# Kernel tuning notes

Hardware: AMD Instinct MI355X
Metric: run time of the kernel (lower is better)

The kernel has to match this reference:

```python
import jax, jax.numpy as jnp
import numpy as np
import itertools

COS_THRES = 0.5
TEMP = 0.1
EPS = 1e-06
NUM_MODALS = 3


def _cosine_sim(t1, t2, l1, l2, eps=EPS):
    # t1:[B1,D], t2:[B2,D], l1:[B1,1], l2:[B2,1] -> [B1,B2]
    return jnp.matmul(t1, t2.T) / jnp.maximum(jnp.matmul(l1, l2.T), eps)


def _filtered_infonce(m1, m2, cos_thres=COS_THRES, temp=TEMP, eps=EPS):
    # m1, m2: [B, D]
    B = m1.shape[0]
    l1 = jnp.sqrt(jnp.sum(m1 * m1, axis=-1, keepdims=True))
    l2 = jnp.sqrt(jnp.sum(m2 * m2, axis=-1, keepdims=True))
    cross = _cosine_sim(m1, m2, l1, l2, eps) / temp          # [B,B] logits
    s1 = _cosine_sim(m1, m1, l1, l1, eps)
    s2 = _cosine_sim(m2, m2, l2, l2, eps)
    mask = (s1 <= cos_thres) | (s2 <= cos_thres)
    mask = mask | jnp.eye(B, dtype=bool)                      # diagonal always kept
    # masked row-wise cross entropy with label i == diagonal.
    # Excluding masked columns then re-indexing the label (torch loop) is
    # equivalent to a masked softmax over the full row with label on the diag.
    neg_inf = jnp.asarray(-jnp.inf, cross.dtype)
    logits = jnp.where(mask, cross, neg_inf)
    lse = jax.nn.logsumexp(logits, axis=-1)                   # [B]
    loss_i = lse - jnp.diagonal(cross)                        # [B]
    valid = jnp.sum(mask, axis=-1) > 1                        # rows with >1 candidates
    count = jnp.sum(valid)
    total = jnp.sum(jnp.where(valid, loss_i, 0.0))
    return jnp.where(count > 0, total / jnp.maximum(count, 1), 0.0)


def setup_inputs() -> dict:
    key = jax.random.key(0)
    all_features = jax.random.normal(key, (NUM_MODALS, 4096, 1024), dtype=jnp.float32)
    return {"all_features": all_features}


def reference(all_features) -> jnp.ndarray:
    # CMCLoss with main_modal_idx=None: InfoNCE over all modal pairs.
    n_modals = all_features.shape[0]
    error = 0.0
    num_components = 0
    for i, j in itertools.combinations(range(n_modals), 2):
        error = error + _filtered_infonce(all_features[i], all_features[j])
        num_components += 1
    return error / num_components
```

## Files before the change

### kernel.cpp

```cpp
#include <hip/hip_runtime.h>
#include <stdint.h>
#include <math.h>

typedef float fx4 __attribute__((ext_vector_type(4)));
typedef float fx16 __attribute__((ext_vector_type(16)));
typedef int   ix4 __attribute__((ext_vector_type(4)));
typedef int   ix8 __attribute__((ext_vector_type(8)));

#define NB 4096
#define ND 1024
#define CEPS 1e-6f
#define CTHR 0.5f
#define NTT 16


__device__ __forceinline__ void gload16(const void* g, void* l) {
  __builtin_amdgcn_global_load_lds(
      (const __attribute__((address_space(1))) uint32_t*)(uintptr_t)g,
      (__attribute__((address_space(3))) uint32_t*)(uint32_t)(uintptr_t)l,
      16, 0, 0);
}

__device__ __forceinline__ ix8 ldfrag8(const char* p0, const char* p1) {
  const ix4 lo = *(const ix4*)p0;
  const ix4 hi = *(const ix4*)p1;
  ix8 r;
  r[0] = lo[0]; r[1] = lo[1]; r[2] = lo[2]; r[3] = lo[3];
  r[4] = hi[0]; r[5] = hi[1]; r[6] = hi[2]; r[7] = hi[3];
  return r;
}

#define MFMAS(A, B, C) \
  __builtin_amdgcn_mfma_scale_f32_32x32x64_f8f6f4((A), (B), (C), 0, 0, 0, 127, 0, 127)


__global__ __launch_bounds__(256) void cmc_convert(
    const float* __restrict__ in, uint8_t* __restrict__ xf8,
    float* __restrict__ lnorm) {
  const int row = blockIdx.x;
  const int tid = threadIdx.x;
  const fx4 v = *(const fx4*)(in + (size_t)row * ND + tid * 4);
  int pk = __builtin_amdgcn_cvt_pk_fp8_f32(v[0], v[1], 0, false);
  pk = __builtin_amdgcn_cvt_pk_fp8_f32(v[2], v[3], pk, true);
  ((int*)(xf8 + (size_t)row * ND))[tid] = pk;
  float ss = v[0]*v[0] + v[1]*v[1] + v[2]*v[2] + v[3]*v[3];
  #pragma unroll
  for (int d = 1; d < 64; d <<= 1) ss += __shfl_xor(ss, d);
  __shared__ float sred[4];
  if ((tid & 63) == 0) sred[tid >> 6] = ss;
  __syncthreads();
  if (tid == 0) lnorm[row] = sqrtf(sred[0] + sred[1] + sred[2] + sred[3]);
}


__device__ __forceinline__ void gram128_f8(
    const uint8_t* __restrict__ Xi, const uint8_t* __restrict__ Xj,
    int rb, int cb, char* smem, int tid, fx16 (&acc)[2][2]) {
  const int l = tid & 63, w = tid >> 6;
  const int wr = w >> 1, wc = w & 1;
  const int srow = tid >> 2;
  const int scol = (((tid & 3) ^ ((tid >> 3) & 3)) << 4);
  const uint8_t* gA0 = Xi + (size_t)(rb + srow) * ND + scol;
  const uint8_t* gA1 = Xi + (size_t)(rb + 64 + srow) * ND + scol;
  const uint8_t* gB0 = Xj + (size_t)(cb + srow) * ND + scol;
  const uint8_t* gB1 = Xj + (size_t)(cb + 64 + srow) * ND + scol;
  char* dA0 = smem + tid * 16;
  char* dA1 = smem + 4096 + tid * 16;
  char* dB0 = smem + 8192 + tid * 16;
  char* dB1 = smem + 12288 + tid * 16;

  const int swzl = ((l >> 1) & 3) << 4;
  const int kb = (l >> 5) * 32;
  const int c0 = kb ^ swzl;
  const int c1 = (kb + 16) ^ swzl;
  const char* rdA = smem + (wr * 64 + (l & 31)) * 64;
  const char* rdB = smem + 8192 + (wc * 64 + (l & 31)) * 64;

  #pragma unroll
  for (int m = 0; m < 2; ++m)
    #pragma unroll
    for (int n = 0; n < 2; ++n)
      #pragma unroll
      for (int e = 0; e < 16; ++e) acc[m][n][e] = 0.f;

  #pragma unroll 1
  for (int t = 0; t < NTT; ++t) {
    const int k0 = t * 64;
    gload16(gA0 + k0, dA0);
    gload16(gA1 + k0, dA1);
    gload16(gB0 + k0, dB0);
    gload16(gB1 + k0, dB1);
    __syncthreads();
    ix8 A[2], B[2];
    #pragma unroll
    for (int m = 0; m < 2; ++m)
      A[m] = ldfrag8(rdA + m * 2048 + c0, rdA + m * 2048 + c1);
    #pragma unroll
    for (int n = 0; n < 2; ++n)
      B[n] = ldfrag8(rdB + n * 2048 + c0, rdB + n * 2048 + c1);
    #pragma unroll
    for (int m = 0; m < 2; ++m)
      #pragma unroll
      for (int n = 0; n < 2; ++n)
        acc[m][n] = MFMAS(A[m], B[n], acc[m][n]);
    __syncthreads();
  }
}


__global__ __launch_bounds__(256, 3) void cmc_selfmask(
    const uint8_t* __restrict__ xf8, const float* __restrict__ lnorm,
    uint32_t* __restrict__ maskw) {
  __shared__ __align__(16) char smem[16384];
  const int md = blockIdx.z;
  const int bx = blockIdx.x, by = blockIdx.y;
  if (by > bx) return;
  const int rb = by * 128, cb = bx * 128;
  const int tid = threadIdx.x;
  const int l = tid & 63, w = tid >> 6;
  const int wr = w >> 1, wc = w & 1;

  const uint8_t* X = xf8 + (size_t)md * NB * ND;
  fx16 acc[2][2];
  gram128_f8(X, X, rb, cb, smem, tid, acc);

  uint32_t* tile = (uint32_t*)smem;
  float* Lr = (float*)(smem + 2048);
  float* Lc = (float*)(smem + 2560 + 512);
  if (tid < 128) {
    Lr[tid] = lnorm[md * NB + rb + tid];
    Lc[tid] = lnorm[md * NB + cb + tid];
  }
  __syncthreads();

  #pragma unroll
  for (int m = 0; m < 2; ++m)
    #pragma unroll
    for (int r = 0; r < 16; ++r) {
      const int rl0 = wr * 64 + m * 32 + (r & 3) + 8 * (r >> 2);
      const float Lrv = Lr[rl0 + 4 * (l >> 5)];
      #pragma unroll
      for (int n = 0; n < 2; ++n) {
        const int cl = wc * 64 + n * 32 + (l & 31);
        const float cv = acc[m][n][r] / fmaxf(Lrv * Lc[cl], CEPS);
        const uint64_t b = __ballot(cv <= CTHR);
        if (l == 0)  tile[(rl0 + 0) * 4 + wc * 2 + n] = (uint32_t)b;
        if (l == 32) tile[(rl0 + 4) * 4 + wc * 2 + n] = (uint32_t)(b >> 32);
      }
    }
  __syncthreads();

  for (int t = tid; t < 512; t += 256) {
    const int row = t >> 2, wd = t & 3;
    maskw[((size_t)md * NB + rb + row) * 128 + (cb >> 5) + wd] = tile[t];
  }
  if (by != bx) {
    for (int t = tid; t < 512; t += 256) {
      const int crow = t & 127;
      const int wp = t >> 7;
      uint32_t wv = 0;
      #pragma unroll
      for (int r = 0; r < 32; ++r) {
        const uint32_t bit = (tile[(wp * 32 + r) * 4 + (crow >> 5)] >> (crow & 31)) & 1u;
        wv |= bit << r;
      }
      maskw[((size_t)md * NB + cb + crow) * 128 + (rb >> 5) + wp] = wv;
    }
  }
}


__global__ __launch_bounds__(256, 3) void cmc_pair(
    const uint8_t* __restrict__ xf8, const float* __restrict__ lnorm,
    const uint32_t* __restrict__ maskw,
    float* __restrict__ sumexp, float* __restrict__ diagv) {
  __shared__ __align__(16) char smem[16384];
  const int p = blockIdx.z;
  const int mi = (p == 2) ? 1 : 0;
  const int mj = (p == 0) ? 1 : 2;
  const int rb = blockIdx.y * 128;
  const int cb = blockIdx.x * 128;
  const int tid = threadIdx.x;
  const int l = tid & 63, w = tid >> 6;
  const int wr = w >> 1, wc = w & 1;

  const uint8_t* Xi = xf8 + (size_t)mi * NB * ND;
  const uint8_t* Xj = xf8 + (size_t)mj * NB * ND;

  fx16 acc[2][2];
  gram128_f8(Xi, Xj, rb, cb, smem, tid, acc);

  uint32_t* Mt = (uint32_t*)smem;
  float* Lri = (float*)(smem + 4096);
  float* Lcj = (float*)(smem + 4608 + 512);
  for (int t = tid; t < 512; t += 256) {
    const int row = t >> 2, wd = t & 3;
    Mt[t]       = maskw[((size_t)mi * NB + rb + row) * 128 + (cb >> 5) + wd];
    Mt[512 + t] = maskw[((size_t)mj * NB + rb + row) * 128 + (cb >> 5) + wd];
  }
  if (tid < 128) {
    Lri[tid] = lnorm[mi * NB + rb + tid];
    Lcj[tid] = lnorm[mj * NB + cb + tid];
  }
  __syncthreads();

  #pragma unroll
  for (int m = 0; m < 2; ++m)
    #pragma unroll
    for (int r = 0; r < 16; ++r) {
      const int rl = wr * 64 + m * 32 + (r & 3) + 8 * (r >> 2) + 4 * (l >> 5);
      const int rg = rb + rl;
      const float Lrv = Lri[rl];
      float se = 0.f;
      #pragma unroll
      for (int n = 0; n < 2; ++n) {
        const int cl = wc * 64 + n * 32 + (l & 31);
        const int cg = cb + cl;
        const uint32_t bi = (Mt[rl * 4 + (cl >> 5)] >> (cl & 31)) & 1u;
        const uint32_t bj = (Mt[512 + rl * 4 + (cl >> 5)] >> (cl & 31)) & 1u;
        const bool msk = bi | bj | (rg == cg);
        const float logit = acc[m][n][r] / fmaxf(Lrv * Lcj[cl], CEPS) * 10.0f;
        if (rg == cg) diagv[p * NB + rg] = logit;
        if (msk) se += __expf(logit);
      }
      #pragma unroll
      for (int d = 1; d < 32; d <<= 1) se += __shfl_xor(se, d);
      if ((l & 31) == 0) atomicAdd(&sumexp[p * NB + rg], se);
    }
}


__global__ __launch_bounds__(256) void cmc_count(
    const uint32_t* __restrict__ maskw, float* __restrict__ cntrow) {
  const int wid = (blockIdx.x * 256 + threadIdx.x) >> 6;
  const int l = threadIdx.x & 63;
  const int p = wid >> 12;
  const int r = wid & 4095;
  const int mi = (p == 2) ? 1 : 0;
  const int mj = (p == 0) ? 1 : 2;
  int cnt = 0;
  #pragma unroll
  for (int h = 0; h < 2; ++h) {
    const int wd = h * 64 + l;
    uint32_t v = maskw[((size_t)mi * NB + r) * 128 + wd] |
                 maskw[((size_t)mj * NB + r) * 128 + wd];
    if ((r >> 5) == wd) v |= (1u << (r & 31));
    cnt += __popc(v);
  }
  #pragma unroll
  for (int d = 1; d < 64; d <<= 1) cnt += __shfl_xor(cnt, d);
  if (l == 0) cntrow[p * NB + r] = (float)cnt;
}


__global__ __launch_bounds__(256) void cmc_final(
    const float* __restrict__ sumexp, const float* __restrict__ cntrow,
    const float* __restrict__ diagv, float* __restrict__ out) {
  const int tid = threadIdx.x;
  __shared__ float sred[8];
  float lsum = 0.f;
  for (int p = 0; p < 3; ++p) {
    float t = 0.f, c = 0.f;
    for (int r = tid; r < NB; r += 256) {
      const float cnt = cntrow[p * NB + r];
      if (cnt > 1.0f) {
        t += logf(sumexp[p * NB + r]) - diagv[p * NB + r];
        c += 1.f;
      }
    }
    #pragma unroll
    for (int d = 1; d < 64; d <<= 1) { t += __shfl_xor(t, d); c += __shfl_xor(c, d); }
    if ((tid & 63) == 0) { sred[(tid >> 6) * 2] = t; sred[(tid >> 6) * 2 + 1] = c; }
    __syncthreads();
    if (tid == 0) {
      const float tt = sred[0] + sred[2] + sred[4] + sred[6];
      const float cc = sred[1] + sred[3] + sred[5] + sred[7];
      lsum += (cc > 0.f) ? tt / fmaxf(cc, 1.f) : 0.f;
    }
    __syncthreads();
  }
  if (tid == 0) out[0] = lsum / 3.0f;
}


extern "C" void kernel_launch(void* const* d_in, const int* in_sizes, int n_in,
                              void* d_out, int out_size, void* d_ws, size_t ws_size,
                              hipStream_t stream) {
  const float* in = (const float*)d_in[0];
  float* out = (float*)d_out;
  char* ws = (char*)d_ws;

  const size_t X8_BYTES = (size_t)3 * NB * ND;
  uint8_t* xf8  = (uint8_t*)ws;
  float* lnorm  = (float*)(ws + X8_BYTES);
  float* sumexp = lnorm + 3 * NB;
  float* cntrow = sumexp + 3 * NB;
  float* diagv  = cntrow + 3 * NB;
  uint32_t* maskw = (uint32_t*)(diagv + 3 * NB);

  hipMemsetAsync(sumexp, 0, (size_t)3 * NB * sizeof(float), stream);

  cmc_convert<<<3 * NB, 256, 0, stream>>>(in, xf8, lnorm);
  cmc_selfmask<<<dim3(NB / 128, NB / 128, 3), 256, 0, stream>>>(xf8, lnorm, maskw);
  cmc_pair<<<dim3(NB / 128, NB / 128, 3), 256, 0, stream>>>(xf8, lnorm, maskw, sumexp, diagv);
  cmc_count<<<3 * NB / 4, 256, 0, stream>>>(maskw, cntrow);
  cmc_final<<<1, 256, 0, stream>>>(sumexp, cntrow, diagv, out);
}
```

Baseline: 241.8 us.

## Use 2-wave blocks with 2x4 MFMA tiles and 128-deep K steps

Rewrites the FP8 Gram tile routine so each 128x128 block uses two waves instead of four. Each wave computes a 64x128 sub-tile (2x4 MFMA accumulators), and each K step loads 128 bytes per row with an 8-way XOR swizzle instead of 64. The aim is more register-level reuse of fragments, half as many barrier iterations, and fewer LDS reads per MFMA. The cost is 32KB of shared memory per block, more accumulator registers, and fewer waves available to hide memory latency.

```diff
diff --git a/kernel.cpp b/kernel.cpp
--- a/kernel.cpp
+++ b/kernel.cpp
@@ -11,7 +11,7 @@
 #define ND 1024
 #define CEPS 1e-6f
 #define CTHR 0.5f
-#define NTT 16
+#define NT8 8
 
 
 __device__ __forceinline__ void gload16(const void* g, void* l) {
@@ -53,80 +53,78 @@
 }
 
 
-__device__ __forceinline__ void gram128_f8(
+__device__ __forceinline__ void gram128B(
     const uint8_t* __restrict__ Xi, const uint8_t* __restrict__ Xj,
-    int rb, int cb, char* smem, int tid, fx16 (&acc)[2][2]) {
+    int rb, int cb, char* smem, int tid, fx16 (&acc)[2][4]) {
   const int l = tid & 63, w = tid >> 6;
-  const int wr = w >> 1, wc = w & 1;
-  const int srow = tid >> 2;
-  const int scol = (((tid & 3) ^ ((tid >> 3) & 3)) << 4);
-  const uint8_t* gA0 = Xi + (size_t)(rb + srow) * ND + scol;
-  const uint8_t* gA1 = Xi + (size_t)(rb + 64 + srow) * ND + scol;
-  const uint8_t* gB0 = Xj + (size_t)(cb + srow) * ND + scol;
-  const uint8_t* gB1 = Xj + (size_t)(cb + 64 + srow) * ND + scol;
-  char* dA0 = smem + tid * 16;
-  char* dA1 = smem + 4096 + tid * 16;
-  char* dB0 = smem + 8192 + tid * 16;
-  char* dB1 = smem + 12288 + tid * 16;
-
-  const int swzl = ((l >> 1) & 3) << 4;
+  const int srow = tid >> 3;
+  const int scol = ((tid & 7) ^ (srow & 7)) << 4;
+  const uint8_t* gA = Xi + (size_t)(rb + srow) * ND + scol;
+  const uint8_t* gB = Xj + (size_t)(cb + srow) * ND + scol;
+  char* dA = smem + tid * 16;
+  char* dB = smem + 16384 + tid * 16;
+
+  const int swz = (l & 7) << 4;
   const int kb = (l >> 5) * 32;
-  const int c0 = kb ^ swzl;
-  const int c1 = (kb + 16) ^ swzl;
-  const char* rdA = smem + (wr * 64 + (l & 31)) * 64;
-  const char* rdB = smem + 8192 + (wc * 64 + (l & 31)) * 64;
+  const char* rdA = smem + (w * 64 + (l & 31)) * 128;
+  const char* rdB = smem + 16384 + (l & 31) * 128;
 
   #pragma unroll
   for (int m = 0; m < 2; ++m)
     #pragma unroll
-    for (int n = 0; n < 2; ++n)
+    for (int n = 0; n < 4; ++n)
       #pragma unroll
       for (int e = 0; e < 16; ++e) acc[m][n][e] = 0.f;
 
   #pragma unroll 1
-  for (int t = 0; t < NTT; ++t) {
-    const int k0 = t * 64;
-    gload16(gA0 + k0, dA0);
-    gload16(gA1 + k0, dA1);
-    gload16(gB0 + k0, dB0);
-    gload16(gB1 + k0, dB1);
+  for (int t = 0; t < NT8; ++t) {
+    const int k0 = t * 128;
+    #pragma unroll
+    for (int s = 0; s < 8; ++s) {
+      gload16(gA + (size_t)s * 16 * ND + k0, dA + s * 2048);
+      gload16(gB + (size_t)s * 16 * ND + k0, dB + s * 2048);
+    }
     __syncthreads();
-    ix8 A[2], B[2];
-    #pragma unroll
-    for (int m = 0; m < 2; ++m)
-      A[m] = ldfrag8(rdA + m * 2048 + c0, rdA + m * 2048 + c1);
-    #pragma unroll
-    for (int n = 0; n < 2; ++n)
-      B[n] = ldfrag8(rdB + n * 2048 + c0, rdB + n * 2048 + c1);
-    #pragma unroll
-    for (int m = 0; m < 2; ++m)
-      #pragma unroll
-      for (int n = 0; n < 2; ++n)
-        acc[m][n] = MFMAS(A[m], B[n], acc[m][n]);
+    #pragma unroll
+    for (int ks = 0; ks < 2; ++ks) {
+      const int c0 = (ks * 64 + kb) ^ swz;
+      const int c1 = (ks * 64 + kb + 16) ^ swz;
+      ix8 A[2], B[4];
+      #pragma unroll
+      for (int m = 0; m < 2; ++m)
+        A[m] = ldfrag8(rdA + m * 4096 + c0, rdA + m * 4096 + c1);
+      #pragma unroll
+      for (int n = 0; n < 4; ++n)
+        B[n] = ldfrag8(rdB + n * 4096 + c0, rdB + n * 4096 + c1);
+      #pragma unroll
+      for (int m = 0; m < 2; ++m)
+        #pragma unroll
+        for (int n = 0; n < 4; ++n)
+          acc[m][n] = MFMAS(A[m], B[n], acc[m][n]);
+    }
     __syncthreads();
   }
 }
 
 
-__global__ __launch_bounds__(256, 3) void cmc_selfmask(
+__global__ __launch_bounds__(128, 2) void cmc_selfmask(
     const uint8_t* __restrict__ xf8, const float* __restrict__ lnorm,
     uint32_t* __restrict__ maskw) {
-  __shared__ __align__(16) char smem[16384];
+  __shared__ __align__(16) char smem[32768];
   const int md = blockIdx.z;
   const int bx = blockIdx.x, by = blockIdx.y;
   if (by > bx) return;
   const int rb = by * 128, cb = bx * 128;
   const int tid = threadIdx.x;
   const int l = tid & 63, w = tid >> 6;
-  const int wr = w >> 1, wc = w & 1;
 
   const uint8_t* X = xf8 + (size_t)md * NB * ND;
-  fx16 acc[2][2];
-  gram128_f8(X, X, rb, cb, smem, tid, acc);
+  fx16 acc[2][4];
+  gram128B(X, X, rb, cb, smem, tid, acc);
 
   uint32_t* tile = (uint32_t*)smem;
   float* Lr = (float*)(smem + 2048);
-  float* Lc = (float*)(smem + 2560 + 512);
+  float* Lc = (float*)(smem + 2560);
   if (tid < 128) {
     Lr[tid] = lnorm[md * NB + rb + tid];
     Lc[tid] = lnorm[md * NB + cb + tid];
@@ -137,25 +135,25 @@
   for (int m = 0; m < 2; ++m)
     #pragma unroll
     for (int r = 0; r < 16; ++r) {
-      const int rl0 = wr * 64 + m * 32 + (r & 3) + 8 * (r >> 2);
+      const int rl0 = w * 64 + m * 32 + (r & 3) + 8 * (r >> 2);
       const float Lrv = Lr[rl0 + 4 * (l >> 5)];
       #pragma unroll
-      for (int n = 0; n < 2; ++n) {
-        const int cl = wc * 64 + n * 32 + (l & 31);
+      for (int n = 0; n < 4; ++n) {
+        const int cl = n * 32 + (l & 31);
         const float cv = acc[m][n][r] / fmaxf(Lrv * Lc[cl], CEPS);
         const uint64_t b = __ballot(cv <= CTHR);
-        if (l == 0)  tile[(rl0 + 0) * 4 + wc * 2 + n] = (uint32_t)b;
-        if (l == 32) tile[(rl0 + 4) * 4 + wc * 2 + n] = (uint32_t)(b >> 32);
+        if (l == 0)  tile[(rl0 + 0) * 4 + n] = (uint32_t)b;
+        if (l == 32) tile[(rl0 + 4) * 4 + n] = (uint32_t)(b >> 32);
       }
     }
   __syncthreads();
 
-  for (int t = tid; t < 512; t += 256) {
+  for (int t = tid; t < 512; t += 128) {
     const int row = t >> 2, wd = t & 3;
     maskw[((size_t)md * NB + rb + row) * 128 + (cb >> 5) + wd] = tile[t];
   }
   if (by != bx) {
-    for (int t = tid; t < 512; t += 256) {
+    for (int t = tid; t < 512; t += 128) {
       const int crow = t & 127;
       const int wp = t >> 7;
       uint32_t wv = 0;
@@ -170,11 +168,11 @@
 }
 
 
-__global__ __launch_bounds__(256, 3) void cmc_pair(
+__global__ __launch_bounds__(128, 2) void cmc_pair(
     const uint8_t* __restrict__ xf8, const float* __restrict__ lnorm,
     const uint32_t* __restrict__ maskw,
     float* __restrict__ sumexp, float* __restrict__ diagv) {
-  __shared__ __align__(16) char smem[16384];
+  __shared__ __align__(16) char smem[32768];
   const int p = blockIdx.z;
   const int mi = (p == 2) ? 1 : 0;
   const int mj = (p == 0) ? 1 : 2;
@@ -182,18 +180,17 @@
   const int cb = blockIdx.x * 128;
   const int tid = threadIdx.x;
   const int l = tid & 63, w = tid >> 6;
-  const int wr = w >> 1, wc = w & 1;
 
   const uint8_t* Xi = xf8 + (size_t)mi * NB * ND;
   const uint8_t* Xj = xf8 + (size_t)mj * NB * ND;
 
-  fx16 acc[2][2];
-  gram128_f8(Xi, Xj, rb, cb, smem, tid, acc);
+  fx16 acc[2][4];
+  gram128B(Xi, Xj, rb, cb, smem, tid, acc);
 
   uint32_t* Mt = (uint32_t*)smem;
   float* Lri = (float*)(smem + 4096);
-  float* Lcj = (float*)(smem + 4608 + 512);
-  for (int t = tid; t < 512; t += 256) {
+  float* Lcj = (float*)(smem + 4608);
+  for (int t = tid; t < 512; t += 128) {
     const int row = t >> 2, wd = t & 3;
     Mt[t]       = maskw[((size_t)mi * NB + rb + row) * 128 + (cb >> 5) + wd];
     Mt[512 + t] = maskw[((size_t)mj * NB + rb + row) * 128 + (cb >> 5) + wd];
@@ -208,13 +205,13 @@
   for (int m = 0; m < 2; ++m)
     #pragma unroll
     for (int r = 0; r < 16; ++r) {
-      const int rl = wr * 64 + m * 32 + (r & 3) + 8 * (r >> 2) + 4 * (l >> 5);
+      const int rl = w * 64 + m * 32 + (r & 3) + 8 * (r >> 2) + 4 * (l >> 5);
       const int rg = rb + rl;
       const float Lrv = Lri[rl];
       float se = 0.f;
       #pragma unroll
-      for (int n = 0; n < 2; ++n) {
-        const int cl = wc * 64 + n * 32 + (l & 31);
+      for (int n = 0; n < 4; ++n) {
+        const int cl = n * 32 + (l & 31);
         const int cg = cb + cl;
         const uint32_t bi = (Mt[rl * 4 + (cl >> 5)] >> (cl & 31)) & 1u;
         const uint32_t bj = (Mt[512 + rl * 4 + (cl >> 5)] >> (cl & 31)) & 1u;
@@ -301,8 +298,8 @@
   hipMemsetAsync(sumexp, 0, (size_t)3 * NB * sizeof(float), stream);
 
   cmc_convert<<<3 * NB, 256, 0, stream>>>(in, xf8, lnorm);
-  cmc_selfmask<<<dim3(NB / 128, NB / 128, 3), 256, 0, stream>>>(xf8, lnorm, maskw);
-  cmc_pair<<<dim3(NB / 128, NB / 128, 3), 256, 0, stream>>>(xf8, lnorm, maskw, sumexp, diagv);
+  cmc_selfmask<<<dim3(NB / 128, NB / 128, 3), 128, 0, stream>>>(xf8, lnorm, maskw);
+  cmc_pair<<<dim3(NB / 128, NB / 128, 3), 128, 0, stream>>>(xf8, lnorm, maskw, sumexp, diagv);
   cmc_count<<<3 * NB / 4, 256, 0, stream>>>(maskw, cntrow);
   cmc_final<<<1, 256, 0, stream>>>(sumexp, cntrow, diagv, out);
 }
```

Result: slower. 251.4 us (+4.0%).

## Double-buffer FP8 gram tiles with 128-wide K steps and fold row counts into pair kernel

Applied to the files above, without the earlier changes.

The gram routine now stages 128-byte K slices in a double-buffered 64 KB LDS region. It prefetches the next slice with global_load_lds while MFMAs run on the current one, and needs only one barrier per iteration. The goal is to hide global-load latency and halve the loop trip count. Occupancy is lowered to 2 blocks per CU to fit the larger LDS. The separate count kernel is removed: cmc_pair now accumulates the masked-column count per row with atomics alongside sumexp, which saves a launch and a reread of the mask.

```diff
diff --git a/kernel.cpp b/kernel.cpp
--- a/kernel.cpp
+++ b/kernel.cpp
@@ -11,7 +11,7 @@
 #define ND 1024
 #define CEPS 1e-6f
 #define CTHR 0.5f
-#define NTT 16
+#define NT8 8
 
 
 __device__ __forceinline__ void gload16(const void* g, void* l) {
@@ -53,28 +53,22 @@
 }
 
 
-__device__ __forceinline__ void gram128_f8(
+__device__ __forceinline__ void gram128D(
     const uint8_t* __restrict__ Xi, const uint8_t* __restrict__ Xj,
     int rb, int cb, char* smem, int tid, fx16 (&acc)[2][2]) {
   const int l = tid & 63, w = tid >> 6;
   const int wr = w >> 1, wc = w & 1;
-  const int srow = tid >> 2;
-  const int scol = (((tid & 3) ^ ((tid >> 3) & 3)) << 4);
-  const uint8_t* gA0 = Xi + (size_t)(rb + srow) * ND + scol;
-  const uint8_t* gA1 = Xi + (size_t)(rb + 64 + srow) * ND + scol;
-  const uint8_t* gB0 = Xj + (size_t)(cb + srow) * ND + scol;
-  const uint8_t* gB1 = Xj + (size_t)(cb + 64 + srow) * ND + scol;
-  char* dA0 = smem + tid * 16;
-  char* dA1 = smem + 4096 + tid * 16;
-  char* dB0 = smem + 8192 + tid * 16;
-  char* dB1 = smem + 12288 + tid * 16;
-
-  const int swzl = ((l >> 1) & 3) << 4;
+  const int srow = tid >> 3;
+  const int scol = (((tid & 7) ^ ((tid >> 3) & 7)) << 4);
+  const uint8_t* gA = Xi + (size_t)(rb + srow) * ND + scol;
+  const uint8_t* gB = Xj + (size_t)(cb + srow) * ND + scol;
+  char* dA = smem + tid * 16;
+  char* dB = smem + 16384 + tid * 16;
+
+  const int swz = (l & 7) << 4;
   const int kb = (l >> 5) * 32;
-  const int c0 = kb ^ swzl;
-  const int c1 = (kb + 16) ^ swzl;
-  const char* rdA = smem + (wr * 64 + (l & 31)) * 64;
-  const char* rdB = smem + 8192 + (wc * 64 + (l & 31)) * 64;
+  const char* rdA = smem + (wr * 64 + (l & 31)) * 128;
+  const char* rdB = smem + 16384 + (wc * 64 + (l & 31)) * 128;
 
   #pragma unroll
   for (int m = 0; m < 2; ++m)
@@ -83,35 +77,54 @@
       #pragma unroll
       for (int e = 0; e < 16; ++e) acc[m][n][e] = 0.f;
 
+  #pragma unroll
+  for (int s = 0; s < 4; ++s) {
+    gload16(gA + (size_t)s * 32 * ND, dA + s * 4096);
+    gload16(gB + (size_t)s * 32 * ND, dB + s * 4096);
+  }
+  asm volatile("s_waitcnt vmcnt(0)" ::: "memory");
+  __builtin_amdgcn_s_barrier();
+
+  int cur = 0;
   #pragma unroll 1
-  for (int t = 0; t < NTT; ++t) {
-    const int k0 = t * 64;
-    gload16(gA0 + k0, dA0);
-    gload16(gA1 + k0, dA1);
-    gload16(gB0 + k0, dB0);
-    gload16(gB1 + k0, dB1);
-    __syncthreads();
-    ix8 A[2], B[2];
-    #pragma unroll
-    for (int m = 0; m < 2; ++m)
-      A[m] = ldfrag8(rdA + m * 2048 + c0, rdA + m * 2048 + c1);
-    #pragma unroll
-    for (int n = 0; n < 2; ++n)
-      B[n] = ldfrag8(rdB + n * 2048 + c0, rdB + n * 2048 + c1);
-    #pragma unroll
-    for (int m = 0; m < 2; ++m)
-      #pragma unroll
-      for (int n = 0; n < 2; ++n)
-        acc[m][n] = MFMAS(A[m], B[n], acc[m][n]);
-    __syncthreads();
-  }
-}
-
-
-__global__ __launch_bounds__(256, 3) void cmc_selfmask(
+  for (int t = 0; t < NT8; ++t) {
+    const int nxt = cur ^ 1;
+    if (t + 1 < NT8) {
+      const int k1 = (t + 1) * 128;
+      #pragma unroll
+      for (int s = 0; s < 4; ++s) {
+        gload16(gA + (size_t)s * 32 * ND + k1, dA + nxt * 32768 + s * 4096);
+        gload16(gB + (size_t)s * 32 * ND + k1, dB + nxt * 32768 + s * 4096);
+      }
+    }
+    const char* bA = rdA + cur * 32768;
+    const char* bB = rdB + cur * 32768;
+    #pragma unroll
+    for (int ks = 0; ks < 2; ++ks) {
+      const int c0 = (ks * 64 + kb) ^ swz;
+      const int c1 = (ks * 64 + kb + 16) ^ swz;
+      ix8 A[2], B[2];
+      A[0] = ldfrag8(bA + c0,        bA + c1);
+      A[1] = ldfrag8(bA + 4096 + c0, bA + 4096 + c1);
+      B[0] = ldfrag8(bB + c0,        bB + c1);
+      B[1] = ldfrag8(bB + 4096 + c0, bB + 4096 + c1);
+      acc[0][0] = MFMAS(A[0], B[0], acc[0][0]);
+      acc[0][1] = MFMAS(A[0], B[1], acc[0][1]);
+      acc[1][0] = MFMAS(A[1], B[0], acc[1][0]);
+      acc[1][1] = MFMAS(A[1], B[1], acc[1][1]);
+    }
+    asm volatile("s_waitcnt lgkmcnt(0)" ::: "memory");
+    asm volatile("s_waitcnt vmcnt(0)" ::: "memory");
+    __builtin_amdgcn_s_barrier();
+    cur = nxt;
+  }
+}
+
+
+__global__ __launch_bounds__(256, 2) void cmc_selfmask(
     const uint8_t* __restrict__ xf8, const float* __restrict__ lnorm,
     uint32_t* __restrict__ maskw) {
-  __shared__ __align__(16) char smem[16384];
+  __shared__ __align__(16) char smem[65536];
   const int md = blockIdx.z;
   const int bx = blockIdx.x, by = blockIdx.y;
   if (by > bx) return;
@@ -122,11 +135,12 @@
 
   const uint8_t* X = xf8 + (size_t)md * NB * ND;
   fx16 acc[2][2];
-  gram128_f8(X, X, rb, cb, smem, tid, acc);
+  gram128D(X, X, rb, cb, smem, tid, acc);
+  __syncthreads();
 
   uint32_t* tile = (uint32_t*)smem;
   float* Lr = (float*)(smem + 2048);
-  float* Lc = (float*)(smem + 2560 + 512);
+  float* Lc = (float*)(smem + 2560);
   if (tid < 128) {
     Lr[tid] = lnorm[md * NB + rb + tid];
     Lc[tid] = lnorm[md * NB + cb + tid];
@@ -170,11 +184,12 @@
 }
 
 
-__global__ __launch_bounds__(256, 3) void cmc_pair(
+__global__ __launch_bounds__(256, 2) void cmc_pair(
     const uint8_t* __restrict__ xf8, const float* __restrict__ lnorm,
     const uint32_t* __restrict__ maskw,
-    float* __restrict__ sumexp, float* __restrict__ diagv) {
-  __shared__ __align__(16) char smem[16384];
+    float* __restrict__ sumexp, float* __restrict__ cntrow,
+    float* __restrict__ diagv) {
+  __shared__ __align__(16) char smem[65536];
   const int p = blockIdx.z;
   const int mi = (p == 2) ? 1 : 0;
   const int mj = (p == 0) ? 1 : 2;
@@ -188,11 +203,12 @@
   const uint8_t* Xj = xf8 + (size_t)mj * NB * ND;
 
   fx16 acc[2][2];
-  gram128_f8(Xi, Xj, rb, cb, smem, tid, acc);
+  gram128D(Xi, Xj, rb, cb, smem, tid, acc);
+  __syncthreads();
 
   uint32_t* Mt = (uint32_t*)smem;
   float* Lri = (float*)(smem + 4096);
-  float* Lcj = (float*)(smem + 4608 + 512);
+  float* Lcj = (float*)(smem + 4608);
   for (int t = tid; t < 512; t += 256) {
     const int row = t >> 2, wd = t & 3;
     Mt[t]       = maskw[((size_t)mi * NB + rb + row) * 128 + (cb >> 5) + wd];
@@ -211,7 +227,7 @@
       const int rl = wr * 64 + m * 32 + (r & 3) + 8 * (r >> 2) + 4 * (l >> 5);
       const int rg = rb + rl;
       const float Lrv = Lri[rl];
-      float se = 0.f;
+      float se = 0.f, ct = 0.f;
       #pragma unroll
       for (int n = 0; n < 2; ++n) {
         const int cl = wc * 64 + n * 32 + (l & 31);
@@ -221,35 +237,18 @@
         const bool msk = bi | bj | (rg == cg);
         const float logit = acc[m][n][r] / fmaxf(Lrv * Lcj[cl], CEPS) * 10.0f;
         if (rg == cg) diagv[p * NB + rg] = logit;
-        if (msk) se += __expf(logit);
-      }
-      #pragma unroll
-      for (int d = 1; d < 32; d <<= 1) se += __shfl_xor(se, d);
-      if ((l & 31) == 0) atomicAdd(&sumexp[p * NB + rg], se);
-    }
-}
-
-
-__global__ __launch_bounds__(256) void cmc_count(
-    const uint32_t* __restrict__ maskw, float* __restrict__ cntrow) {
-  const int wid = (blockIdx.x * 256 + threadIdx.x) >> 6;
-  const int l = threadIdx.x & 63;
-  const int p = wid >> 12;
-  const int r = wid & 4095;
-  const int mi = (p == 2) ? 1 : 0;
-  const int mj = (p == 0) ? 1 : 2;
-  int cnt = 0;
-  #pragma unroll
-  for (int h = 0; h < 2; ++h) {
-    const int wd = h * 64 + l;
-    uint32_t v = maskw[((size_t)mi * NB + r) * 128 + wd] |
-                 maskw[((size_t)mj * NB + r) * 128 + wd];
-    if ((r >> 5) == wd) v |= (1u << (r & 31));
-    cnt += __popc(v);
-  }
-  #pragma unroll
-  for (int d = 1; d < 64; d <<= 1) cnt += __shfl_xor(cnt, d);
-  if (l == 0) cntrow[p * NB + r] = (float)cnt;
+        if (msk) { se += __expf(logit); ct += 1.f; }
+      }
+      #pragma unroll
+      for (int d = 1; d < 32; d <<= 1) {
+        se += __shfl_xor(se, d);
+        ct += __shfl_xor(ct, d);
+      }
+      if ((l & 31) == 0) {
+        atomicAdd(&sumexp[p * NB + rg], se);
+        atomicAdd(&cntrow[p * NB + rg], ct);
+      }
+    }
 }
 
 
@@ -298,11 +297,10 @@
   float* diagv  = cntrow + 3 * NB;
   uint32_t* maskw = (uint32_t*)(diagv + 3 * NB);
 
-  hipMemsetAsync(sumexp, 0, (size_t)3 * NB * sizeof(float), stream);
+  hipMemsetAsync(sumexp, 0, (size_t)2 * 3 * NB * sizeof(float), stream);
 
   cmc_convert<<<3 * NB, 256, 0, stream>>>(in, xf8, lnorm);
   cmc_selfmask<<<dim3(NB / 128, NB / 128, 3), 256, 0, stream>>>(xf8, lnorm, maskw);
-  cmc_pair<<<dim3(NB / 128, NB / 128, 3), 256, 0, stream>>>(xf8, lnorm, maskw, sumexp, diagv);
-  cmc_count<<<3 * NB / 4, 256, 0, stream>>>(maskw, cntrow);
+  cmc_pair<<<dim3(NB / 128, NB / 128, 3), 256, 0, stream>>>(xf8, lnorm, maskw, sumexp, cntrow, diagv);
   cmc_final<<<1, 256, 0, stream>>>(sumexp, cntrow, diagv, out);
 }
```

Result: slower. 304.4 us (+25.9%).
